# Kernel optimization log

Measured on AMD Instinct MI355X. Metric: run time of the kernel, lower is better.

Reference implementation:

```python
import jax, jax.numpy as jnp
import numpy as np

HEADS = 12
DIM = 768
DH = DIM // HEADS


def setup_inputs() -> dict:
    key = jax.random.key(0)
    k1, k2 = jax.random.split(key)
    z = jax.random.normal(k1, (4, 2048, DIM), dtype=jnp.float32)
    # nn.Linear(dim, 3*dim, bias=False): weight shape [3*dim, dim], y = z @ W.T
    W_qkv = jax.random.normal(k2, (3 * DIM, DIM), dtype=jnp.float32) * (1.0 / np.sqrt(DIM))
    return {"z": z, "W_qkv": W_qkv}


def reference(z, W_qkv):
    b, n, d = z.shape
    qkv = jnp.einsum('bnd,ed->bne', z, W_qkv)  # [b, n, 3*dim]
    # last dim layout is (headNum, m, Dh) per the einops pattern '(headNum m Dh)'
    qkv = qkv.reshape(b, n, HEADS, 3, DH)
    q = jnp.transpose(qkv[:, :, :, 0, :], (0, 2, 1, 3))  # [b, h, n, Dh]
    k = jnp.transpose(qkv[:, :, :, 1, :], (0, 2, 1, 3))
    v = jnp.transpose(qkv[:, :, :, 2, :], (0, 2, 1, 3))
    scores = jnp.einsum('bhqd,bhkd->bhqk', q, k) / np.sqrt(DH).astype(np.float32)
    A = jax.nn.softmax(scores, axis=-1)  # full [b, h, n, n] matrix, as in source
    out = jnp.einsum('bhqk,bhkd->bhqd', A, v)  # [b, h, n, Dh]
    return jnp.transpose(out, (0, 2, 1, 3)).reshape(b, n, d)
```

## Files before the change

kernel.cpp:

```cpp
#include <hip/hip_runtime.h>
#include <hip/hip_bf16.h>
#include <stdint.h>


typedef __attribute__((ext_vector_type(8))) short bf8_t;
typedef __attribute__((ext_vector_type(4))) float f4_t;

__device__ __forceinline__ unsigned short f2bf(float f) {
  union { float f; unsigned u; } x; x.f = f;
  return (unsigned short)((x.u + 0x7fffu + ((x.u >> 16) & 1u)) >> 16);
}
__device__ __forceinline__ unsigned cvt_pk_bf16(float lo, float hi) {
  unsigned r;
  asm("v_cvt_pk_bf16_f32 %0, %1, %2" : "=v"(r) : "v"(lo), "v"(hi));
  return r;
}
__device__ __forceinline__ void gload_lds16(const void* g, void* l) {
  __builtin_amdgcn_global_load_lds(
      (const __attribute__((address_space(1))) void*)g,
      (__attribute__((address_space(3))) void*)l, 16, 0, 0);
}

__global__ __launch_bounds__(256) void cvt_kernel(
    const float* __restrict__ Z, const float* __restrict__ W,
    unsigned short* __restrict__ Zb)
{
  const int idx = blockIdx.x * 256 + threadIdx.x;
  const float* src;
  unsigned short* dst;
  int c;
  if (idx < 786432) { src = Z; dst = Zb; c = idx; }
  else              { src = W; dst = Zb + 6291456; c = idx - 786432; }
  const float4 a0 = *(const float4*)(src + (size_t)c * 8);
  const float4 a1 = *(const float4*)(src + (size_t)c * 8 + 4);
  uint4 pk = { cvt_pk_bf16(a0.x, a0.y), cvt_pk_bf16(a0.z, a0.w),
               cvt_pk_bf16(a1.x, a1.y), cvt_pk_bf16(a1.z, a1.w) };
  *(uint4*)(dst + (size_t)c * 8) = pk;
}

__global__ __launch_bounds__(256, 3) void qkv_gemm_kernel(
    const unsigned short* __restrict__ Zb, const unsigned short* __restrict__ Wb,
    unsigned short* __restrict__ qb, unsigned short* __restrict__ kb,
    unsigned short* __restrict__ vt)
{
  __shared__ __align__(16) unsigned short As[128 * 64];
  __shared__ __align__(16) unsigned short Bs[128 * 64];

  const int tid = threadIdx.x;
  const int w    = tid >> 6;
  const int lane = tid & 63;
  const int g    = lane >> 4;
  const int l15  = lane & 15;
  const int bid0 = blockIdx.y * 18 + blockIdx.x;
  const int bid  = (bid0 & 7) * 144 + (bid0 >> 3);
  const int m0 = (bid / 18) * 128;
  const int n0 = (bid % 18) * 128;
  const int wr = w >> 1, wc = w & 1;

  const int arow = w * 32 + (lane >> 3);
  const int achk = ((lane & 7) ^ (lane >> 3)) * 8;
  const unsigned short* za = Zb + (size_t)(m0 + arow) * 768 + achk;
  const unsigned short* wa = Wb + (size_t)(n0 + arow) * 768 + achk;
  unsigned short* const lza = As + w * 32 * 64;
  unsigned short* const lwa = Bs + w * 32 * 64;

  const f4_t zf = {0.f, 0.f, 0.f, 0.f};
  f4_t acc[4][4];
#pragma unroll
  for (int m = 0; m < 4; ++m)
#pragma unroll
    for (int n = 0; n < 4; ++n) acc[m][n] = zf;

  for (int ks = 0; ks < 12; ++ks) {
    __syncthreads();
#pragma unroll
    for (int r = 0; r < 4; ++r) {
      gload_lds16(za + r * 8 * 768, lza + r * 512);
      gload_lds16(wa + r * 8 * 768, lwa + r * 512);
    }
    za += 64; wa += 64;
    __syncthreads();

#pragma unroll
    for (int s = 0; s < 2; ++s) {
      bf8_t af[4], bfr[4];
#pragma unroll
      for (int m = 0; m < 4; ++m) {
        const int row = wr * 64 + m * 16 + l15;
        af[m] = *(const bf8_t*)(As + row * 64 + (((s * 4 + g) ^ (row & 7)) * 8));
      }
#pragma unroll
      for (int n = 0; n < 4; ++n) {
        const int row = wc * 64 + n * 16 + l15;
        bfr[n] = *(const bf8_t*)(Bs + row * 64 + (((s * 4 + g) ^ (row & 7)) * 8));
      }
      __builtin_amdgcn_s_setprio(1);
#pragma unroll
      for (int m = 0; m < 4; ++m)
#pragma unroll
        for (int n = 0; n < 4; ++n)
          acc[m][n] = __builtin_amdgcn_mfma_f32_16x16x32_bf16(af[m], bfr[n], acc[m][n], 0, 0, 0);
      __builtin_amdgcn_s_setprio(0);
    }
  }

  const float QSCALE = 0.18033688011112042f;
#pragma unroll
  for (int m = 0; m < 4; ++m) {
    const int gi  = m0 + wr * 64 + m * 16 + g * 4;
    const int b   = gi >> 11;
    const int tok = gi & 2047;
#pragma unroll
    for (int n = 0; n < 4; ++n) {
      const int e0  = n0 + wc * 64 + n * 16;
      const int h   = e0 / 192;
      const int rem = e0 - h * 192;
      const int mm  = rem >> 6;
      const int dh  = (rem & 63) + l15;
      if (mm == 2) {
        uint2 pk = { cvt_pk_bf16(acc[m][n][0], acc[m][n][1]),
                     cvt_pk_bf16(acc[m][n][2], acc[m][n][3]) };
        const int pos = ((tok >> 5) & 1) * 32 + ((tok >> 2) & 3) * 8
                      + ((tok >> 4) & 1) * 4;
        const size_t vaddr = ((size_t)(b * 12 + h) * 32 + (tok >> 6)) * 4096
                           + dh * 64 + pos;
        *(uint2*)(vt + vaddr) = pk;
      } else {
        unsigned short* buf = mm ? kb : qb;
        const float sc = mm ? 1.0f : QSCALE;
        const size_t base = ((size_t)((b * 12 + h) * 2048 + tok)) * 64 + dh;
#pragma unroll
        for (int j = 0; j < 4; ++j)
          buf[base + (size_t)j * 64] = f2bf(acc[m][n][j] * sc);
      }
    }
  }
}

__global__ __launch_bounds__(256, 3) void attn_kernel(
    const unsigned short* __restrict__ qb, const unsigned short* __restrict__ kb,
    const unsigned short* __restrict__ vt, float* __restrict__ out)
{
  __shared__ __align__(16) unsigned short Ks[2][64 * 64];
  __shared__ __align__(16) unsigned short Vs[2][64 * 64];

  const int bid = blockIdx.x;
  const int nb  = (bid & 7) * 96 + (bid >> 3);
  const int bh  = nb >> 4;
  const int qt  = nb & 15;
  const int tid = threadIdx.x;
  const int w    = tid >> 6;
  const int lane = tid & 63;
  const int g    = lane >> 4;
  const int l15  = lane & 15;

  const unsigned short* Qh  = qb + (size_t)bh * 2048 * 64;
  const unsigned short* Kh  = kb + (size_t)bh * 2048 * 64;
  const unsigned short* VTh = vt + (size_t)bh * 32 * 4096;

  const int qbase = qt * 128 + w * 32;

  bf8_t qfr[2][2];
#pragma unroll
  for (int qq = 0; qq < 2; ++qq)
#pragma unroll
    for (int s = 0; s < 2; ++s)
      qfr[qq][s] = *(const bf8_t*)(Qh + (size_t)(qbase + qq * 16 + l15) * 64 + s * 32 + g * 8);

  const size_t dmaoff = (size_t)(w * 16 + (lane >> 3)) * 64
                      + ((lane & 7) ^ (lane >> 3)) * 8;
  const unsigned short* ksrc = Kh + dmaoff;
  const unsigned short* vsrc = VTh + dmaoff;
  const int ldsoff = w * 16 * 64;

  gload_lds16(ksrc,          &Ks[0][ldsoff]);
  gload_lds16(ksrc + 8 * 64, &Ks[0][ldsoff + 8 * 64]);
  gload_lds16(vsrc,          &Vs[0][ldsoff]);
  gload_lds16(vsrc + 8 * 64, &Vs[0][ldsoff + 8 * 64]);
  __syncthreads();

  const f4_t zf  = {0.f, 0.f, 0.f, 0.f};
  const f4_t m16 = {-16.f, -16.f, -16.f, -16.f};
  f4_t accO[2][4];
  float lsum[2] = {0.f, 0.f};
#pragma unroll
  for (int qq = 0; qq < 2; ++qq)
#pragma unroll
    for (int nf = 0; nf < 4; ++nf) accO[qq][nf] = zf;

  for (int t = 0; t < 32; ++t) {
    const int cur = t & 1, nxt = cur ^ 1;
    const unsigned short* KsC = Ks[cur];
    const unsigned short* VsC = Vs[cur];

    if (t < 31) {
      const unsigned short* kn = ksrc + (size_t)(t + 1) * 4096;
      const unsigned short* vn = vsrc + (size_t)(t + 1) * 4096;
      gload_lds16(kn,          &Ks[nxt][ldsoff]);
      gload_lds16(kn + 8 * 64, &Ks[nxt][ldsoff + 8 * 64]);
      gload_lds16(vn,          &Vs[nxt][ldsoff]);
      gload_lds16(vn + 8 * 64, &Vs[nxt][ldsoff + 8 * 64]);
    }

    bf8_t ka[4][2];
#pragma unroll
    for (int kf = 0; kf < 4; ++kf) {
      const int row = kf * 16 + l15;
#pragma unroll
      for (int s = 0; s < 2; ++s)
        ka[kf][s] = *(const bf8_t*)(KsC + row * 64 + (((s * 4 + g) ^ (row & 7)) * 8));
    }
    f4_t accS[4][2];
    __builtin_amdgcn_s_setprio(1);
#pragma unroll
    for (int kf = 0; kf < 4; ++kf)
#pragma unroll
      for (int qq = 0; qq < 2; ++qq) {
        f4_t a = __builtin_amdgcn_mfma_f32_16x16x32_bf16(ka[kf][0], qfr[qq][0], m16, 0, 0, 0);
        a = __builtin_amdgcn_mfma_f32_16x16x32_bf16(ka[kf][1], qfr[qq][1], a, 0, 0, 0);
        accS[kf][qq] = a;
      }
    __builtin_amdgcn_s_setprio(0);

    bf8_t vfr[2][4];
#pragma unroll
    for (int kk = 0; kk < 2; ++kk)
#pragma unroll
      for (int nf = 0; nf < 4; ++nf) {
        const int dh = nf * 16 + l15;
        vfr[kk][nf] = *(const bf8_t*)(VsC + dh * 64 + (((4 * kk + g) ^ (dh & 7)) * 8));
      }

    bf8_t pa[2][2];
#pragma unroll
    for (int qq = 0; qq < 2; ++qq) {
      union { bf8_t v[2]; unsigned uw[8]; } P8;
      float ps = 0.f;
#pragma unroll
      for (int kf = 0; kf < 4; ++kf) {
        const float p0 = __builtin_amdgcn_exp2f(accS[kf][qq][0]);
        const float p1 = __builtin_amdgcn_exp2f(accS[kf][qq][1]);
        const float p2 = __builtin_amdgcn_exp2f(accS[kf][qq][2]);
        const float p3 = __builtin_amdgcn_exp2f(accS[kf][qq][3]);
        ps += (p0 + p1) + (p2 + p3);
        P8.uw[kf * 2]     = cvt_pk_bf16(p0, p1);
        P8.uw[kf * 2 + 1] = cvt_pk_bf16(p2, p3);
      }
      ps += __shfl_xor(ps, 16);
      ps += __shfl_xor(ps, 32);
      lsum[qq] += ps;
      pa[qq][0] = P8.v[0];
      pa[qq][1] = P8.v[1];
    }

    __builtin_amdgcn_s_setprio(1);
#pragma unroll
    for (int kk = 0; kk < 2; ++kk)
#pragma unroll
      for (int nf = 0; nf < 4; ++nf)
#pragma unroll
        for (int qq = 0; qq < 2; ++qq)
          accO[qq][nf] = __builtin_amdgcn_mfma_f32_16x16x32_bf16(pa[qq][kk], vfr[kk][nf], accO[qq][nf], 0, 0, 0);
    __builtin_amdgcn_s_setprio(0);

    __syncthreads();
  }

  const int b = bh / 12, h = bh - (bh / 12) * 12;
#pragma unroll
  for (int qq = 0; qq < 2; ++qq) {
    const float rl = 1.0f / lsum[qq];
    f4_t lv;
#pragma unroll
    for (int j = 0; j < 4; ++j) lv[j] = __shfl(rl, g * 4 + j);
#pragma unroll
    for (int nf = 0; nf < 4; ++nf) {
#pragma unroll
      for (int j = 0; j < 4; ++j) {
        const int qrow = qbase + qq * 16 + g * 4 + j;
        out[((size_t)(b * 2048 + qrow)) * 768 + h * 64 + nf * 16 + l15] = accO[qq][nf][j] * lv[j];
      }
    }
  }
}

extern "C" void kernel_launch(void* const* d_in, const int* in_sizes, int n_in,
                              void* d_out, int out_size, void* d_ws, size_t ws_size,
                              hipStream_t stream) {
  (void)in_sizes; (void)n_in; (void)out_size; (void)ws_size;
  const float* Z = (const float*)d_in[0];
  const float* W = (const float*)d_in[1];
  float* out = (float*)d_out;

  unsigned short* qb = (unsigned short*)d_ws;
  unsigned short* kb = qb + (size_t)48 * 2048 * 64;
  unsigned short* vt = kb + (size_t)48 * 2048 * 64;

  unsigned short* Zb = (unsigned short*)d_out;
  unsigned short* Wb = Zb + (size_t)8192 * 768;

  cvt_kernel<<<dim3(3936), 256, 0, stream>>>(Z, W, Zb);
  qkv_gemm_kernel<<<dim3(18, 64), 256, 0, stream>>>(Zb, Wb, qb, kb, vt);
  attn_kernel<<<dim3(768), 256, 0, stream>>>(qb, kb, vt, out);
}
```

Before: 112.7 us.

## Prefetch K/V two tiles ahead and interleave softmax with PV MFMAs

The K/V tile loads now run two iterations ahead. Each iteration reads its fragments from LDS into registers, hits a barrier, and then refills the same buffer with tile t+2, so global latency gets more time to hide behind compute. The softmax of one query subtile is also interleaved with the PV MFMAs of the other, which lets exp work overlap with matrix ops. The barrier now sits mid-iteration rather than at the end, and the prologue loads two tiles up front.

```diff
diff --git a/kernel.cpp b/kernel.cpp
--- a/kernel.cpp
+++ b/kernel.cpp
@@ -173,10 +173,14 @@
   const unsigned short* vsrc = VTh + dmaoff;
   const int ldsoff = w * 16 * 64;
 
-  gload_lds16(ksrc,          &Ks[0][ldsoff]);
-  gload_lds16(ksrc + 8 * 64, &Ks[0][ldsoff + 8 * 64]);
-  gload_lds16(vsrc,          &Vs[0][ldsoff]);
-  gload_lds16(vsrc + 8 * 64, &Vs[0][ldsoff + 8 * 64]);
+  gload_lds16(ksrc,                 &Ks[0][ldsoff]);
+  gload_lds16(ksrc + 8 * 64,        &Ks[0][ldsoff + 8 * 64]);
+  gload_lds16(vsrc,                 &Vs[0][ldsoff]);
+  gload_lds16(vsrc + 8 * 64,        &Vs[0][ldsoff + 8 * 64]);
+  gload_lds16(ksrc + 4096,          &Ks[1][ldsoff]);
+  gload_lds16(ksrc + 4096 + 8 * 64, &Ks[1][ldsoff + 8 * 64]);
+  gload_lds16(vsrc + 4096,          &Vs[1][ldsoff]);
+  gload_lds16(vsrc + 4096 + 8 * 64, &Vs[1][ldsoff + 8 * 64]);
   __syncthreads();
 
   const f4_t zf  = {0.f, 0.f, 0.f, 0.f};
@@ -189,19 +193,10 @@
     for (int nf = 0; nf < 4; ++nf) accO[qq][nf] = zf;
 
   for (int t = 0; t < 32; ++t) {
-    const int cur = t & 1, nxt = cur ^ 1;
+    const int cur = t & 1;
     const unsigned short* KsC = Ks[cur];
     const unsigned short* VsC = Vs[cur];
 
-    if (t < 31) {
-      const unsigned short* kn = ksrc + (size_t)(t + 1) * 4096;
-      const unsigned short* vn = vsrc + (size_t)(t + 1) * 4096;
-      gload_lds16(kn,          &Ks[nxt][ldsoff]);
-      gload_lds16(kn + 8 * 64, &Ks[nxt][ldsoff + 8 * 64]);
-      gload_lds16(vn,          &Vs[nxt][ldsoff]);
-      gload_lds16(vn + 8 * 64, &Vs[nxt][ldsoff + 8 * 64]);
-    }
-
     bf8_t ka[4][2];
 #pragma unroll
     for (int kf = 0; kf < 4; ++kf) {
@@ -210,18 +205,6 @@
       for (int s = 0; s < 2; ++s)
         ka[kf][s] = *(const bf8_t*)(KsC + row * 64 + (((s * 4 + g) ^ (row & 7)) * 8));
     }
-    f4_t accS[4][2];
-    __builtin_amdgcn_s_setprio(1);
-#pragma unroll
-    for (int kf = 0; kf < 4; ++kf)
-#pragma unroll
-      for (int qq = 0; qq < 2; ++qq) {
-        f4_t a = __builtin_amdgcn_mfma_f32_16x16x32_bf16(ka[kf][0], qfr[qq][0], m16, 0, 0, 0);
-        a = __builtin_amdgcn_mfma_f32_16x16x32_bf16(ka[kf][1], qfr[qq][1], a, 0, 0, 0);
-        accS[kf][qq] = a;
-      }
-    __builtin_amdgcn_s_setprio(0);
-
     bf8_t vfr[2][4];
 #pragma unroll
     for (int kk = 0; kk < 2; ++kk)
@@ -231,17 +214,42 @@
         vfr[kk][nf] = *(const bf8_t*)(VsC + dh * 64 + (((4 * kk + g) ^ (dh & 7)) * 8));
       }
 
-    bf8_t pa[2][2];
+    __syncthreads();
+
+    if (t < 30) {
+      const unsigned short* kn = ksrc + (size_t)(t + 2) * 4096;
+      const unsigned short* vn = vsrc + (size_t)(t + 2) * 4096;
+      gload_lds16(kn,          &Ks[cur][ldsoff]);
+      gload_lds16(kn + 8 * 64, &Ks[cur][ldsoff + 8 * 64]);
+      gload_lds16(vn,          &Vs[cur][ldsoff]);
+      gload_lds16(vn + 8 * 64, &Vs[cur][ldsoff + 8 * 64]);
+    }
+
+    f4_t accS0[4], accS1[4];
+    __builtin_amdgcn_s_setprio(1);
+#pragma unroll
+    for (int kf = 0; kf < 4; ++kf) {
+      f4_t a = __builtin_amdgcn_mfma_f32_16x16x32_bf16(ka[kf][0], qfr[0][0], m16, 0, 0, 0);
+      accS0[kf] = __builtin_amdgcn_mfma_f32_16x16x32_bf16(ka[kf][1], qfr[0][1], a, 0, 0, 0);
+    }
+#pragma unroll
+    for (int kf = 0; kf < 4; ++kf) {
+      f4_t a = __builtin_amdgcn_mfma_f32_16x16x32_bf16(ka[kf][0], qfr[1][0], m16, 0, 0, 0);
+      accS1[kf] = __builtin_amdgcn_mfma_f32_16x16x32_bf16(ka[kf][1], qfr[1][1], a, 0, 0, 0);
+    }
+    __builtin_amdgcn_s_setprio(0);
+
 #pragma unroll
     for (int qq = 0; qq < 2; ++qq) {
+      const f4_t* accS = qq ? accS1 : accS0;
       union { bf8_t v[2]; unsigned uw[8]; } P8;
       float ps = 0.f;
 #pragma unroll
       for (int kf = 0; kf < 4; ++kf) {
-        const float p0 = __builtin_amdgcn_exp2f(accS[kf][qq][0]);
-        const float p1 = __builtin_amdgcn_exp2f(accS[kf][qq][1]);
-        const float p2 = __builtin_amdgcn_exp2f(accS[kf][qq][2]);
-        const float p3 = __builtin_amdgcn_exp2f(accS[kf][qq][3]);
+        const float p0 = __builtin_amdgcn_exp2f(accS[kf][0]);
+        const float p1 = __builtin_amdgcn_exp2f(accS[kf][1]);
+        const float p2 = __builtin_amdgcn_exp2f(accS[kf][2]);
+        const float p3 = __builtin_amdgcn_exp2f(accS[kf][3]);
         ps += (p0 + p1) + (p2 + p3);
         P8.uw[kf * 2]     = cvt_pk_bf16(p0, p1);
         P8.uw[kf * 2 + 1] = cvt_pk_bf16(p2, p3);
@@ -249,21 +257,15 @@
       ps += __shfl_xor(ps, 16);
       ps += __shfl_xor(ps, 32);
       lsum[qq] += ps;
-      pa[qq][0] = P8.v[0];
-      pa[qq][1] = P8.v[1];
-    }
-
-    __builtin_amdgcn_s_setprio(1);
-#pragma unroll
-    for (int kk = 0; kk < 2; ++kk)
-#pragma unroll
-      for (int nf = 0; nf < 4; ++nf)
-#pragma unroll
-        for (int qq = 0; qq < 2; ++qq)
-          accO[qq][nf] = __builtin_amdgcn_mfma_f32_16x16x32_bf16(pa[qq][kk], vfr[kk][nf], accO[qq][nf], 0, 0, 0);
-    __builtin_amdgcn_s_setprio(0);
-
-    __syncthreads();
+
+      __builtin_amdgcn_s_setprio(1);
+#pragma unroll
+      for (int kk = 0; kk < 2; ++kk)
+#pragma unroll
+        for (int nf = 0; nf < 4; ++nf)
+          accO[qq][nf] = __builtin_amdgcn_mfma_f32_16x16x32_bf16(P8.v[kk], vfr[kk][nf], accO[qq][nf], 0, 0, 0);
+      __builtin_amdgcn_s_setprio(0);
+    }
   }
 
   const int b = bh / 12, h = bh - (bh / 12) * 12;
```

Result: no change. 110.5 us (-1.9%).
